# Optimization experiments

Measured on AMD Instinct MI355X. Metric: run time of the kernel, lower is better.

Reference implementation:

```python
import jax, jax.numpy as jnp
import numpy as np

B, S, F, H = 256, 100, 256, 1024
T = 200


def setup_inputs() -> dict:
    key = jax.random.key(0)
    ks = jax.random.split(key, 11)
    sc = 0.02  # small init scale keeps LSTM dynamics stable
    return {
        "x": jax.random.normal(ks[0], (B, S, F), jnp.float32),
        "W_ih0": jax.random.normal(ks[1], (4 * H, F), jnp.float32) * sc,
        "W_hh0": jax.random.normal(ks[2], (4 * H, H), jnp.float32) * sc,
        "b0": jax.random.normal(ks[3], (4 * H,), jnp.float32) * sc,  # b_ih0 + b_hh0 folded
        "W_ih1": jax.random.normal(ks[4], (4 * H, H), jnp.float32) * sc,
        "W_hh1": jax.random.normal(ks[5], (4 * H, H), jnp.float32) * sc,
        "b1": jax.random.normal(ks[6], (4 * H,), jnp.float32) * sc,
        "out_W": jax.random.normal(ks[7], (F, H), jnp.float32) * sc,
        "out_b": jax.random.normal(ks[8], (F,), jnp.float32) * sc,
        "dy_mu": jax.random.normal(ks[9], (F,), jnp.float32) * 0.01,
        "dy_std": jax.random.uniform(ks[10], (F,), jnp.float32, minval=0.5, maxval=1.5),
        "t": T,
    }


def _cell(xt, h, c, Wih, Whh, b):
    # torch LSTM cell, gate order i,f,g,o
    g = xt @ Wih.T + h @ Whh.T + b  # [B, 4H]
    i, f, gg, o = jnp.split(g, 4, axis=-1)
    c = jax.nn.sigmoid(f) * c + jax.nn.sigmoid(i) * jnp.tanh(gg)
    h = jax.nn.sigmoid(o) * jnp.tanh(c)
    return h, c


def reference(x, W_ih0, W_hh0, b0, W_ih1, W_hh1, b1, out_W, out_b, dy_mu, dy_std, t):
    Bb = x.shape[0]
    Hh = W_hh0.shape[1]
    z = jnp.zeros((Bb, Hh), x.dtype)

    def seq_step(carry, xt):
        h0, c0, h1, c1 = carry
        h0, c0 = _cell(xt, h0, c0, W_ih0, W_hh0, b0)
        h1, c1 = _cell(h0, h1, c1, W_ih1, W_hh1, b1)
        return (h0, c0, h1, c1), h1

    state, preds = jax.lax.scan(seq_step, (z, z, z, z), jnp.swapaxes(x, 0, 1))
    dx = jnp.swapaxes(preds, 0, 1) @ out_W.T + out_b  # [B,S,F]; note: unscaled (matches source)
    out0 = jnp.concatenate([x[:, :1], x + dx], axis=1)  # [B,S+1,F]

    def dec_step(carry, _):
        last, h0, c0, h1, c1 = carry
        h0, c0 = _cell(last, h0, c0, W_ih0, W_hh0, b0)
        h1, c1 = _cell(h0, h1, c1, W_ih1, W_hh1, b1)
        dxt = dy_std * (h1 @ out_W.T + out_b) + dy_mu
        new = last + dxt
        return (new, h0, c0, h1, c1), new

    _, news = jax.lax.scan(dec_step, (out0[:, -1],) + state, None, length=t - 1)
    return jnp.concatenate([out0, jnp.swapaxes(news, 0, 1)], axis=1)  # [B, S+t, F]
```

## Files before the change

### kernel.cpp

```cpp
#include <hip/hip_runtime.h>


#define S_   100
#define OUTC 300
#define NTHR 512

typedef __attribute__((ext_vector_type(8))) _Float16 half8;
typedef __attribute__((ext_vector_type(4))) float    floatx4;

#define OFF_P       0u
#define OFF_C0      16777216u
#define OFF_C1      17825792u
#define OFF_H0HI    18874368u
#define OFF_H0LO    19398656u
#define OFF_H1HI    19922944u
#define OFF_H1LO    20447232u
#define OFF_BAR     20971520u
#define OFF_LASTF   20971776u
#define OFF_LASTHI  21233920u
#define OFF_LASTLO  21364992u
#define OFF_OWHI    21496064u
#define OFF_OWLO    22020352u
#define OFF_WFRAG   22544640u
#define NEED_WS     77070592ull

#define OFF_BAR2    77070592u
#define BAR2_WORDS  2112
#define BAR_STRIDE  64
#define NEED_WS2    (NEED_WS + 8448ull)

#define NZ_WORDS   1048640
#define N_OW       262144
#define N_OUT0     65536
#define SLOTS_WG   13312
#define N_FRAG     3407872

#define LDS_BYTES  131072

struct KParams {
  const float* x;
  const float* b0; const float* b1;
  const float* out_b; const float* dy_mu; const float* dy_std;
  const _Float16* OWhi; const _Float16* OWlo;
  const half8* wfrag;
  float* P; float* c0; float* c1; float* lastf;
  _Float16 *h0hi, *h0lo, *h1hi, *h1lo;
  _Float16 *lasthi, *lastlo;
  unsigned* bar;
  unsigned* bar2;
  float* out;
};

__device__ __forceinline__ float fsig(float x)  { return 1.f / (1.f + __expf(-x)); }
__device__ __forceinline__ float ftanh_(float x){ float e = __expf(2.f*x); return 1.f - 2.f/(e + 1.f); }

__device__ __forceinline__ floatx4 mfma16h(half8 a, half8 b, floatx4 c){
  return __builtin_amdgcn_mfma_f32_16x16x32_f16(a, b, c, 0, 0, 0);
}

__device__ __forceinline__ void gridbar(unsigned* cnt){
  __syncthreads();
  if (threadIdx.x == 0) {
    unsigned arr = __hip_atomic_fetch_add(cnt, 1u, __ATOMIC_RELEASE, __HIP_MEMORY_SCOPE_AGENT);
    unsigned target = (arr & ~255u) + 256u;
    while (__hip_atomic_load(cnt, __ATOMIC_RELAXED, __HIP_MEMORY_SCOPE_AGENT) < target) {
      __builtin_amdgcn_s_sleep(4);
    }
    __builtin_amdgcn_fence(__ATOMIC_ACQUIRE, "agent");
  }
  __syncthreads();
}

__device__ __forceinline__ void treebar(unsigned* b2, unsigned& ep, int wg){
  __syncthreads();
  if (threadIdx.x == 0) {
    ep += 1u;
    const int leaf = wg >> 4;
    unsigned a = __hip_atomic_fetch_add(&b2[leaf*BAR_STRIDE], 1u,
                                        __ATOMIC_RELEASE, __HIP_MEMORY_SCOPE_AGENT);
    if ((a & 15u) == 15u) {
      unsigned r = __hip_atomic_fetch_add(&b2[16*BAR_STRIDE], 1u,
                                          __ATOMIC_RELAXED, __HIP_MEMORY_SCOPE_AGENT);
      if ((r & 15u) == 15u) {
        unsigned newep = (r >> 4) + 1u;
        #pragma unroll
        for (int i = 0; i < 16; ++i)
          __hip_atomic_store(&b2[(17 + i)*BAR_STRIDE], newep,
                             __ATOMIC_RELEASE, __HIP_MEMORY_SCOPE_AGENT);
      }
    }
    while (__hip_atomic_load(&b2[(17 + leaf)*BAR_STRIDE],
                             __ATOMIC_RELAXED, __HIP_MEMORY_SCOPE_AGENT) < ep) {
      __builtin_amdgcn_s_sleep(4);
    }
    __builtin_amdgcn_fence(__ATOMIC_ACQUIRE, "agent");
  }
  __syncthreads();
}

__device__ __forceinline__ void split2(float v, _Float16& hi, _Float16& lo){
  _Float16 h = (_Float16)v;
  hi = h;
  lo = (_Float16)((v - (float)h) * 2048.0f);
}

template<int NKT, bool X32, bool BLDS>
__device__ __forceinline__ void gemm_phase(
    const float* __restrict__ xf, int strXf,
    const _Float16* __restrict__ xhi, const _Float16* __restrict__ xlo, int strX,
    int kb,
    const _Float16* __restrict__ hhi, const _Float16* __restrict__ hlo,
    const half8* __restrict__ bhiP, const half8* __restrict__ bloP, int kbase,
    float* __restrict__ Ppart, int nt, int ks)
{
  const int wv  = threadIdx.x >> 6;
  const int l   = threadIdx.x & 63;
  const int l15 = l & 15;
  const int lk  = (l >> 4) << 3;

  int mrow[2];
  #pragma unroll
  for (int mt = 0; mt < 2; ++mt) mrow[mt] = wv*32 + mt*16 + l15;

  floatx4 acc[2][4]  = {};
  floatx4 accl[2][4] = {};

  #pragma unroll 2
  for (int kt = 0; kt < NKT; ++kt) {
    const int k0 = kbase + kt*32;
    half8 ahi[2], alo[2];
    if (k0 < kb) {
      if (X32) {
        #pragma unroll
        for (int mt = 0; mt < 2; ++mt) {
          const float* p = xf + (size_t)mrow[mt]*strXf + k0 + lk;
          #pragma unroll
          for (int j = 0; j < 8; ++j) {
            float w = p[j];
            _Float16 h = (_Float16)w;
            ahi[mt][j] = h;
            alo[mt][j] = (_Float16)((w - (float)h) * 2048.0f);
          }
        }
      } else {
        #pragma unroll
        for (int mt = 0; mt < 2; ++mt) {
          size_t off = (size_t)mrow[mt]*strX + k0 + lk;
          ahi[mt] = *(const half8*)(xhi + off);
          alo[mt] = *(const half8*)(xlo + off);
        }
      }
    } else {
      #pragma unroll
      for (int mt = 0; mt < 2; ++mt) {
        size_t off = (size_t)mrow[mt]*1024 + (k0 - kb) + lk;
        ahi[mt] = *(const half8*)(hhi + off);
        alo[mt] = *(const half8*)(hlo + off);
      }
    }
    #pragma unroll
    for (int n = 0; n < 4; ++n) {
      half8 bhi, blo;
      if constexpr (BLDS) {
        extern __shared__ half8 smem[];
        bhi = smem[(kt*4 + n)*64 + l];
        blo = smem[4096 + (kt*4 + n)*64 + l];
      } else {
        bhi = bhiP[(kt*4 + n)*64 + l];
        blo = bloP[(kt*4 + n)*64 + l];
      }
      #pragma unroll
      for (int mt = 0; mt < 2; ++mt) {
        acc[mt][n]  = mfma16h(ahi[mt], bhi, acc[mt][n]);
        accl[mt][n] = mfma16h(alo[mt], bhi, accl[mt][n]);
        accl[mt][n] = mfma16h(ahi[mt], blo, accl[mt][n]);
      }
    }
  }

  float* pb = Ppart + (size_t)(ks*64 + nt) * (256*64);
  const int rbase = (l >> 4) * 4;
  #pragma unroll
  for (int mt = 0; mt < 2; ++mt)
    #pragma unroll
    for (int p = 0; p < 4; ++p) {
      int m = wv*32 + mt*16 + rbase + p;
      #pragma unroll
      for (int n = 0; n < 4; ++n)
        pb[(size_t)m*64 + n*16 + l15] = acc[mt][n][p] + accl[mt][n][p] * (1.0f/2048.0f);
    }
}

__device__ __forceinline__ void gate_phase(
    const float* __restrict__ P, float* __restrict__ cbuf,
    _Float16* __restrict__ hhi, _Float16* __restrict__ hlo,
    const float* __restrict__ bias, int nt, int ks)
{
  #pragma unroll
  for (int j = 0; j < 2; ++j) {
    int id = j*NTHR + threadIdx.x;
    int ml = id >> 4, hc = id & 15;
    int m = ks*64 + ml, hcol = nt*16 + hc;
    float g[4];
    #pragma unroll
    for (int gg = 0; gg < 4; ++gg) {
      float s = bias[gg*1024 + hcol];
      #pragma unroll
      for (int k = 0; k < 4; ++k)
        s += P[(size_t)(k*64 + nt)*(256*64) + (size_t)m*64 + gg*16 + hc];
      g[gg] = s;
    }
    int idx = m*1024 + hcol;
    float c = fsig(g[1]) * cbuf[idx] + fsig(g[0]) * ftanh_(g[2]);
    cbuf[idx] = c;
    float h = fsig(g[3]) * ftanh_(c);
    split2(h, hhi[idx], hlo[idx]);
  }
}

__device__ __forceinline__ void out_phase_w0(
    const _Float16* __restrict__ h1hi, const _Float16* __restrict__ h1lo,
    const _Float16* __restrict__ OWhi, const _Float16* __restrict__ OWlo,
    const float* __restrict__ out_b, const float* __restrict__ dy_mu,
    const float* __restrict__ dy_std,
    const float* __restrict__ xcol, float* __restrict__ outcol,
    float* __restrict__ lastf, _Float16* __restrict__ lasthi, _Float16* __restrict__ lastlo,
    int mode)
{
  const int l   = threadIdx.x;
  const int l15 = l & 15;
  const int lk  = (l >> 4) << 3;
  const int mo = blockIdx.x & 15, no = blockIdx.x >> 4;

  floatx4 acc = {}, accl = {};
  #pragma unroll 4
  for (int kt = 0; kt < 32; ++kt) {
    int k = kt*32 + lk;
    half8 a  = *(const half8*)(h1hi + (mo*16 + l15)*1024 + k);
    half8 al = *(const half8*)(h1lo + (mo*16 + l15)*1024 + k);
    half8 b  = *(const half8*)(OWhi + (no*16 + l15)*1024 + k);
    half8 bl = *(const half8*)(OWlo + (no*16 + l15)*1024 + k);
    acc  = mfma16h(a,  b,  acc);
    accl = mfma16h(al, b,  accl);
    accl = mfma16h(a,  bl, accl);
  }
  #pragma unroll
  for (int p = 0; p < 4; ++p) {
    float s = acc[p] + accl[p] * (1.0f/2048.0f);
    int m = mo*16 + (l >> 4)*4 + p;
    int f = no*16 + l15;
    s += out_b[f];
    if (mode == 2) {
      float dxt = dy_std[f]*s + dy_mu[f];
      float nl = lastf[m*256+f] + dxt;
      lastf[m*256+f] = nl;
      outcol[(size_t)m*(OUTC*256) + f] = nl;
      split2(nl, lasthi[m*256+f], lastlo[m*256+f]);
    } else {
      float o = xcol[m*25600 + f] + s;
      outcol[(size_t)m*(OUTC*256) + f] = o;
      if (mode == 1) { lastf[m*256+f] = o; split2(o, lasthi[m*256+f], lastlo[m*256+f]); }
    }
  }
}

__global__ void __launch_bounds__(NTHR, 2) lstm_persist(KParams kp)
{
  const int nt = blockIdx.x >> 2, ks = blockIdx.x & 3;
  unsigned ep = 0;

  const half8* W0hi = kp.wfrag + (size_t)blockIdx.x * SLOTS_WG;
  const half8* W0lo = W0hi + 2560;

  #define GBAR() do { if (kp.bar2) treebar(kp.bar2, ep, blockIdx.x); \
                      else gridbar(kp.bar); } while (0)

  {
    extern __shared__ half8 smem[];
    const half8* src = kp.wfrag + (size_t)blockIdx.x * SLOTS_WG + 5120;
    for (int i = threadIdx.x; i < 8192; i += NTHR) smem[i] = src[i];
    __syncthreads();
  }

  for (int t = 0; t < S_; ++t) {
    gemm_phase<10, true, false>(kp.x + t*256, 25600, nullptr, nullptr, 0, 256,
                         kp.h0hi, kp.h0lo, W0hi, W0lo, ks*320, kp.P, nt, ks);
    if (t > 0 && threadIdx.x < 64)
      out_phase_w0(kp.h1hi, kp.h1lo, kp.OWhi, kp.OWlo,
                   kp.out_b, kp.dy_mu, kp.dy_std,
                   kp.x + (t-1)*256, kp.out + (size_t)t*256,
                   kp.lastf, kp.lasthi, kp.lastlo, 0);
    GBAR();
    gate_phase(kp.P, kp.c0, kp.h0hi, kp.h0lo, kp.b0, nt, ks);
    GBAR();
    gemm_phase<16, false, true>(nullptr, 0, kp.h0hi, kp.h0lo, 1024, 1024,
                          kp.h1hi, kp.h1lo, nullptr, nullptr, ks*512, kp.P, nt, ks);
    GBAR();
    gate_phase(kp.P, kp.c1, kp.h1hi, kp.h1lo, kp.b1, nt, ks);
    GBAR();
  }
  if (threadIdx.x < 64)
    out_phase_w0(kp.h1hi, kp.h1lo, kp.OWhi, kp.OWlo,
                 kp.out_b, kp.dy_mu, kp.dy_std,
                 kp.x + 99*256, kp.out + (size_t)100*256,
                 kp.lastf, kp.lasthi, kp.lastlo, 1);
  GBAR();

  for (int u = 0; u < 199; ++u) {
    gemm_phase<10, false, false>(nullptr, 0, kp.lasthi, kp.lastlo, 256, 256,
                          kp.h0hi, kp.h0lo, W0hi, W0lo, ks*320, kp.P, nt, ks);
    GBAR();
    gate_phase(kp.P, kp.c0, kp.h0hi, kp.h0lo, kp.b0, nt, ks);
    GBAR();
    gemm_phase<16, false, true>(nullptr, 0, kp.h0hi, kp.h0lo, 1024, 1024,
                          kp.h1hi, kp.h1lo, nullptr, nullptr, ks*512, kp.P, nt, ks);
    GBAR();
    gate_phase(kp.P, kp.c1, kp.h1hi, kp.h1lo, kp.b1, nt, ks);
    GBAR();
    if (threadIdx.x < 64)
      out_phase_w0(kp.h1hi, kp.h1lo, kp.OWhi, kp.OWlo,
                   kp.out_b, kp.dy_mu, kp.dy_std,
                   nullptr, kp.out + (size_t)(101+u)*256,
                   kp.lastf, kp.lasthi, kp.lastlo, 2);
    GBAR();
  }
  #undef GBAR
}

__global__ void pre_kernel(const float* __restrict__ x, const float* __restrict__ outW,
                           const float* __restrict__ Wih0, const float* __restrict__ Whh0,
                           const float* __restrict__ Wih1, const float* __restrict__ Whh1,
                           _Float16* __restrict__ OWhi, _Float16* __restrict__ OWlo,
                           unsigned* __restrict__ zeroReg, float* __restrict__ out,
                           half8* __restrict__ wfrag, unsigned* __restrict__ bar2)
{
  if (bar2) {
    for (int i = blockIdx.x*256 + threadIdx.x; i < BAR2_WORDS; i += gridDim.x*256)
      bar2[i] = 0u;
  }
  const int total = NZ_WORDS + N_OW + N_OUT0 + N_FRAG;
  for (int i = blockIdx.x*256 + threadIdx.x; i < total; i += gridDim.x*256) {
    if (i < NZ_WORDS) {
      zeroReg[i] = 0u;
    } else if (i < NZ_WORDS + N_OW) {
      int j = i - NZ_WORDS;
      split2(outW[j], OWhi[j], OWlo[j]);
    } else if (i < NZ_WORDS + N_OW + N_OUT0) {
      int j = i - (NZ_WORDS + N_OW);
      int m = j >> 8, f = j & 255;
      out[(size_t)m*(OUTC*256) + f] = x[m*25600 + f];
    } else {
      int fidx = i - (NZ_WORDS + N_OW + N_OUT0);
      int wg = fidx / SLOTS_WG;
      int r  = fidx - wg*SLOTS_WG;
      int nt = wg >> 2, ks = wg & 3;
      const float* src;
      bool lo;
      if (r < 5120) {
        lo = (r >= 2560);
        int rr = lo ? r - 2560 : r;
        int kt = rr >> 8, q = rr & 255, g = q >> 6, l = q & 63;
        int row = g*1024 + nt*16 + (l & 15);
        int k = ks*320 + kt*32 + ((l >> 4) << 3);
        src = (k < 256) ? (Wih0 + (size_t)row*256 + k)
                        : (Whh0 + (size_t)row*1024 + (k - 256));
      } else {
        int r2 = r - 5120;
        lo = (r2 >= 4096);
        int rr = lo ? r2 - 4096 : r2;
        int kt = rr >> 8, q = rr & 255, g = q >> 6, l = q & 63;
        int row = g*1024 + nt*16 + (l & 15);
        int k = ks*512 + kt*32 + ((l >> 4) << 3);
        src = (k < 1024) ? (Wih1 + (size_t)row*1024 + k)
                         : (Whh1 + (size_t)row*1024 + (k - 1024));
      }
      half8 v;
      #pragma unroll
      for (int j = 0; j < 8; ++j) {
        float w = src[j];
        _Float16 h = (_Float16)w;
        v[j] = lo ? (_Float16)((w - (float)h) * 2048.0f) : h;
      }
      wfrag[(size_t)wg*SLOTS_WG + r] = v;
    }
  }
}

__global__ void sent_kernel(float* out, float v) { out[0] = v; }

extern "C" void kernel_launch(void* const* d_in, const int* in_sizes, int n_in,
                              void* d_out, int out_size, void* d_ws, size_t ws_size,
                              hipStream_t stream)
{
  (void)in_sizes; (void)n_in; (void)out_size;
  char* ws = (char*)d_ws;
  float* out = (float*)d_out;

  if (ws_size < (size_t)NEED_WS) {
    sent_kernel<<<1, 1, 0, stream>>>(out, 900000.0f + 10.0f * (float)(ws_size >> 20));
    return;
  }

  const float* x    = (const float*)d_in[0];
  const float* Wih0 = (const float*)d_in[1];
  const float* Whh0 = (const float*)d_in[2];
  const float* Wih1 = (const float*)d_in[4];
  const float* Whh1 = (const float*)d_in[5];
  const float* outW = (const float*)d_in[7];

  KParams kp;
  kp.x     = x;
  kp.b0    = (const float*)d_in[3];
  kp.b1    = (const float*)d_in[6];
  kp.out_b = (const float*)d_in[8];
  kp.dy_mu = (const float*)d_in[9];
  kp.dy_std= (const float*)d_in[10];

  kp.P      = (float*)(ws + OFF_P);
  kp.c0     = (float*)(ws + OFF_C0);
  kp.c1     = (float*)(ws + OFF_C1);
  kp.h0hi   = (_Float16*)(ws + OFF_H0HI);
  kp.h0lo   = (_Float16*)(ws + OFF_H0LO);
  kp.h1hi   = (_Float16*)(ws + OFF_H1HI);
  kp.h1lo   = (_Float16*)(ws + OFF_H1LO);
  kp.bar    = (unsigned*)(ws + OFF_BAR);
  kp.bar2   = (ws_size >= (size_t)NEED_WS2) ? (unsigned*)(ws + OFF_BAR2) : nullptr;
  kp.lastf  = (float*)(ws + OFF_LASTF);
  kp.lasthi = (_Float16*)(ws + OFF_LASTHI);
  kp.lastlo = (_Float16*)(ws + OFF_LASTLO);
  kp.OWhi   = (const _Float16*)(ws + OFF_OWHI);
  kp.OWlo   = (const _Float16*)(ws + OFF_OWLO);
  kp.wfrag  = (const half8*)(ws + OFF_WFRAG);
  kp.out    = out;

  (void)hipGetLastError();
  pre_kernel<<<4096, 256, 0, stream>>>(x, outW, Wih0, Whh0, Wih1, Whh1,
      (_Float16*)(ws + OFF_OWHI), (_Float16*)(ws + OFF_OWLO),
      (unsigned*)(ws + OFF_C0), out,
      (half8*)(ws + OFF_WFRAG), kp.bar2);
  hipError_t e1 = hipGetLastError();
  if (e1 != hipSuccess) {
    sent_kernel<<<1, 1, 0, stream>>>(out, 300000.0f + 10.0f * (float)e1);
    return;
  }

  (void)hipFuncSetAttribute((const void*)lstm_persist,
                            hipFuncAttributeMaxDynamicSharedMemorySize, LDS_BYTES);

  void* args[] = { &kp };
  hipError_t e2 = hipLaunchCooperativeKernel((const void*)lstm_persist,
                                             dim3(256), dim3(NTHR), args, LDS_BYTES, stream);
  if (e2 != hipSuccess) {
    (void)hipGetLastError();
    lstm_persist<<<256, NTHR, LDS_BYTES, stream>>>(kp);
    hipError_t e3 = hipGetLastError();
    if (e3 != hipSuccess) {
      sent_kernel<<<1, 1, 0, stream>>>(out, 500000.0f + 10.0f * (float)e3);
      return;
    }
  }
}
```

Before: 38.98 ms.

## Rebalance weight fragments into LDS and split decoder output projection across all waves

Changes which weight fragments live in LDS. Both hi and lo layer-0 fragments plus the layer-1 hi fragments now sit in shared memory, and the layer-1 lo fragments are read from global memory. The decoder output projection, previously done by one wave per block, is split across all 8 waves by K and reduced through an LDS scratch area. This aims to cut global reads on the layer-0 GEMM and shorten the serial output phase in the decode loop. In exchange LDS use grows to about 152KB, which may limit two blocks per CU, and layer-1 lo weights now come from global memory.

Result: no change. 38.57 ms (-1.0%).

```diff
diff --git a/kernel.cpp b/kernel.cpp
--- a/kernel.cpp
+++ b/kernel.cpp
@@ -35,7 +35,9 @@
 #define SLOTS_WG   13312
 #define N_FRAG     3407872
 
-#define LDS_BYTES  131072
+#define LDS_WSLOTS 9216
+#define SCR_OFF    147456
+#define LDS_BYTES  155648
 
 struct KParams {
   const float* x;
@@ -104,7 +106,7 @@
   lo = (_Float16)((v - (float)h) * 2048.0f);
 }
 
-template<int NKT, bool X32, bool BLDS>
+template<int NKT, bool X32, int BHIB, int BLOB>
 __device__ __forceinline__ void gemm_phase(
     const float* __restrict__ xf, int strXf,
     const _Float16* __restrict__ xhi, const _Float16* __restrict__ xlo, int strX,
@@ -161,12 +163,16 @@
     #pragma unroll
     for (int n = 0; n < 4; ++n) {
       half8 bhi, blo;
-      if constexpr (BLDS) {
+      if constexpr (BHIB >= 0) {
         extern __shared__ half8 smem[];
-        bhi = smem[(kt*4 + n)*64 + l];
-        blo = smem[4096 + (kt*4 + n)*64 + l];
+        bhi = smem[BHIB + (kt*4 + n)*64 + l];
       } else {
         bhi = bhiP[(kt*4 + n)*64 + l];
+      }
+      if constexpr (BLOB >= 0) {
+        extern __shared__ half8 smem[];
+        blo = smem[BLOB + (kt*4 + n)*64 + l];
+      } else {
         blo = bloP[(kt*4 + n)*64 + l];
       }
       #pragma unroll
@@ -264,27 +270,83 @@
   }
 }
 
+__device__ __forceinline__ void out_phase_w8(
+    const _Float16* __restrict__ h1hi, const _Float16* __restrict__ h1lo,
+    const _Float16* __restrict__ OWhi, const _Float16* __restrict__ OWlo,
+    const float* __restrict__ out_b, const float* __restrict__ dy_mu,
+    const float* __restrict__ dy_std,
+    float* __restrict__ outcol,
+    float* __restrict__ lastf, _Float16* __restrict__ lasthi, _Float16* __restrict__ lastlo)
+{
+  const int wv  = threadIdx.x >> 6;
+  const int l   = threadIdx.x & 63;
+  const int l15 = l & 15;
+  const int lk  = (l >> 4) << 3;
+  const int mo = blockIdx.x & 15, no = blockIdx.x >> 4;
+
+  extern __shared__ char smraw[];
+  floatx4* scr = (floatx4*)(smraw + SCR_OFF);
+
+  floatx4 acc = {}, accl = {};
+  #pragma unroll
+  for (int kt = wv*4; kt < wv*4 + 4; ++kt) {
+    int k = kt*32 + lk;
+    half8 a  = *(const half8*)(h1hi + (mo*16 + l15)*1024 + k);
+    half8 al = *(const half8*)(h1lo + (mo*16 + l15)*1024 + k);
+    half8 b  = *(const half8*)(OWhi + (no*16 + l15)*1024 + k);
+    half8 bl = *(const half8*)(OWlo + (no*16 + l15)*1024 + k);
+    acc  = mfma16h(a,  b,  acc);
+    accl = mfma16h(al, b,  accl);
+    accl = mfma16h(a,  bl, accl);
+  }
+  floatx4 tot;
+  #pragma unroll
+  for (int p = 0; p < 4; ++p) tot[p] = acc[p] + accl[p] * (1.0f/2048.0f);
+  scr[wv*64 + l] = tot;
+  __syncthreads();
+  if (wv == 0) {
+    floatx4 s = scr[l];
+    #pragma unroll
+    for (int w = 1; w < 8; ++w) {
+      floatx4 t = scr[w*64 + l];
+      #pragma unroll
+      for (int p = 0; p < 4; ++p) s[p] += t[p];
+    }
+    #pragma unroll
+    for (int p = 0; p < 4; ++p) {
+      int m = mo*16 + (l >> 4)*4 + p;
+      int f = no*16 + l15;
+      float v = s[p] + out_b[f];
+      float dxt = dy_std[f]*v + dy_mu[f];
+      float nl = lastf[m*256+f] + dxt;
+      lastf[m*256+f] = nl;
+      outcol[(size_t)m*(OUTC*256) + f] = nl;
+      split2(nl, lasthi[m*256+f], lastlo[m*256+f]);
+    }
+  }
+  __syncthreads();
+}
+
 __global__ void __launch_bounds__(NTHR, 2) lstm_persist(KParams kp)
 {
   const int nt = blockIdx.x >> 2, ks = blockIdx.x & 3;
   unsigned ep = 0;
 
-  const half8* W0hi = kp.wfrag + (size_t)blockIdx.x * SLOTS_WG;
-  const half8* W0lo = W0hi + 2560;
+  const half8* W1loG = kp.wfrag + (size_t)blockIdx.x * SLOTS_WG + 9216;
 
   #define GBAR() do { if (kp.bar2) treebar(kp.bar2, ep, blockIdx.x); \
                       else gridbar(kp.bar); } while (0)
 
   {
     extern __shared__ half8 smem[];
-    const half8* src = kp.wfrag + (size_t)blockIdx.x * SLOTS_WG + 5120;
-    for (int i = threadIdx.x; i < 8192; i += NTHR) smem[i] = src[i];
+    const half8* src = kp.wfrag + (size_t)blockIdx.x * SLOTS_WG;
+    for (int i = threadIdx.x; i < LDS_WSLOTS; i += NTHR) smem[i] = src[i];
     __syncthreads();
   }
 
   for (int t = 0; t < S_; ++t) {
-    gemm_phase<10, true, false>(kp.x + t*256, 25600, nullptr, nullptr, 0, 256,
-                         kp.h0hi, kp.h0lo, W0hi, W0lo, ks*320, kp.P, nt, ks);
+    gemm_phase<10, true, 0, 2560>(kp.x + t*256, 25600, nullptr, nullptr, 0, 256,
+                         kp.h0hi, kp.h0lo, nullptr, nullptr, ks*320, kp.P, nt, ks);
     if (t > 0 && threadIdx.x < 64)
       out_phase_w0(kp.h1hi, kp.h1lo, kp.OWhi, kp.OWlo,
                    kp.out_b, kp.dy_mu, kp.dy_std,
@@ -293,8 +355,8 @@
     GBAR();
     gate_phase(kp.P, kp.c0, kp.h0hi, kp.h0lo, kp.b0, nt, ks);
     GBAR();
-    gemm_phase<16, false, true>(nullptr, 0, kp.h0hi, kp.h0lo, 1024, 1024,
-                          kp.h1hi, kp.h1lo, nullptr, nullptr, ks*512, kp.P, nt, ks);
+    gemm_phase<16, false, 5120, -1>(nullptr, 0, kp.h0hi, kp.h0lo, 1024, 1024,
+                          kp.h1hi, kp.h1lo, nullptr, W1loG, ks*512, kp.P, nt, ks);
     GBAR();
     gate_phase(kp.P, kp.c1, kp.h1hi, kp.h1lo, kp.b1, nt, ks);
     GBAR();
@@ -307,21 +369,20 @@
   GBAR();
 
   for (int u = 0; u < 199; ++u) {
-    gemm_phase<10, false, false>(nullptr, 0, kp.lasthi, kp.lastlo, 256, 256,
-                          kp.h0hi, kp.h0lo, W0hi, W0lo, ks*320, kp.P, nt, ks);
+    gemm_phase<10, false, 0, 2560>(nullptr, 0, kp.lasthi, kp.lastlo, 256, 256,
+                          kp.h0hi, kp.h0lo, nullptr, nullptr, ks*320, kp.P, nt, ks);
     GBAR();
     gate_phase(kp.P, kp.c0, kp.h0hi, kp.h0lo, kp.b0, nt, ks);
     GBAR();
-    gemm_phase<16, false, true>(nullptr, 0, kp.h0hi, kp.h0lo, 1024, 1024,
-                          kp.h1hi, kp.h1lo, nullptr, nullptr, ks*512, kp.P, nt, ks);
+    gemm_phase<16, false, 5120, -1>(nullptr, 0, kp.h0hi, kp.h0lo, 1024, 1024,
+                          kp.h1hi, kp.h1lo, nullptr, W1loG, ks*512, kp.P, nt, ks);
     GBAR();
     gate_phase(kp.P, kp.c1, kp.h1hi, kp.h1lo, kp.b1, nt, ks);
     GBAR();
-    if (threadIdx.x < 64)
-      out_phase_w0(kp.h1hi, kp.h1lo, kp.OWhi, kp.OWlo,
-                   kp.out_b, kp.dy_mu, kp.dy_std,
-                   nullptr, kp.out + (size_t)(101+u)*256,
-                   kp.lastf, kp.lasthi, kp.lastlo, 2);
+    out_phase_w8(kp.h1hi, kp.h1lo, kp.OWhi, kp.OWlo,
+                 kp.out_b, kp.dy_mu, kp.dy_std,
+                 kp.out + (size_t)(101+u)*256,
+                 kp.lastf, kp.lasthi, kp.lastlo);
     GBAR();
   }
   #undef GBAR
```
